# Performance work log

Measured on AMD Instinct MI355X. Metric: run time of the kernel, lower is better.

## Reference

```python
import jax, jax.numpy as jnp
import numpy as np
import math

FACTOR = 5


def setup_inputs() -> dict:
    key = jax.random.key(0)
    k1, k2, k3, k4 = jax.random.split(key, 4)
    B, L, H, D = 4, 2048, 8, 64
    sample_k = FACTOR * int(np.ceil(np.log(L)))  # 40
    queries = jax.random.normal(k1, (B, L, H, D), dtype=jnp.float32)
    keys = jax.random.normal(k2, (B, L, H, D), dtype=jnp.float32)
    values = jax.random.normal(k3, (B, L, H, D), dtype=jnp.float32)
    # per-query sampled key indices (replaces the host-side random.sample loop)
    index_sample = jax.random.randint(k4, (L, sample_k), 0, L, dtype=jnp.int64)
    return {"queries": queries, "keys": keys, "values": values,
            "index_sample": index_sample}


def reference(queries, keys, values, index_sample):
    B, L_Q, H, D = queries.shape
    L_K = keys.shape[1]
    # [B, L, H, D] -> [B, H, L, D]
    Q = jnp.transpose(queries, (0, 2, 1, 3))
    K = jnp.transpose(keys, (0, 2, 1, 3))
    V = jnp.transpose(values, (0, 2, 1, 3))

    u = min(FACTOR * int(np.ceil(np.log(L_Q))), L_Q)  # n_top

    # --- _prob_QK: sample-score-topk-gather ---
    # K_sample[b,h,i,s,e] = K[b,h,index_sample[i,s],e]  -> [B,H,L_Q,S,E]
    K_sample = K[:, :, index_sample, :]
    Q_K_sample = jnp.einsum('bhie,bhise->bhis', Q, K_sample)  # [B,H,L_Q,S]
    M = Q_K_sample.max(axis=-1) - Q_K_sample.sum(axis=-1) / L_K  # [B,H,L_Q]
    _, M_top = jax.lax.top_k(M, u)  # [B,H,u] indices of sparse queries

    Q_reduce = jnp.take_along_axis(Q, M_top[..., None], axis=2)  # [B,H,u,D]
    scores = jnp.einsum('bhue,bhke->bhuk', Q_reduce, K)  # [B,H,u,L_K]

    scale = 1.0 / math.sqrt(D)
    scores = scores * scale

    # --- initial context (mask_flag=True): causal running sum of V ---
    context = jnp.cumsum(V, axis=2)  # [B,H,L_Q,D]

    # --- ProbMask: causal mask rows gathered at M_top ---
    causal_mask = jnp.arange(L_K)[None, None, None, :] > M_top[..., None]
    scores = jnp.where(causal_mask, -jnp.inf, scores)
    attn = jax.nn.softmax(scores, axis=-1)  # [B,H,u,L_K]

    update = jnp.einsum('bhuk,bhkd->bhud', attn, V)  # [B,H,u,D]
    bi = jnp.arange(B)[:, None, None]
    hi = jnp.arange(H)[None, :, None]
    context = context.at[bi, hi, M_top].set(update)

    # back to [B, L, H, D]
    return jnp.transpose(context, (0, 2, 1, 3))
```

## Files before the change

kernel.cpp:

```cpp
#include <hip/hip_runtime.h>
#include <hip/hip_bf16.h>
#include <math.h>


#define BB 4
#define LL 2048
#define HH 8
#define DD 64
#define SS 40
#define UU 40
#define CC 64
#define LC (LL/CC)

#define KC    64
#define NCH2  8
#define UG    2
#define KSUB  4
#define KPAD  68
#define PPAD  68

#define NCSB  512
#define NMSB  (BB*LL)
#define NATB  (BB*HH*NCH2*UG)
#define NCUB  512

__global__ void k_measure_cs(const float* __restrict__ Q, const float* __restrict__ K,
                             const float* __restrict__ V, const int* __restrict__ idx,
                             float* __restrict__ M, float* __restrict__ chunkSum)
{
    __shared__ float sMax[4][8];
    __shared__ float sSum[4][8];

    int t = threadIdx.x;

    if (blockIdx.x < NCSB) {
        int w = t >> 6, lane = t & 63;
        int cI = blockIdx.x * 4 + w;
        int bh = cI >> 6, c = cI & (CC - 1);
        int b  = bh >> 3, h = bh & 7;
        int d4 = lane & 15, rs = lane >> 4;

        float4 acc = {0,0,0,0};
        int l0 = c * LC;
        for (int l = l0 + rs; l < l0 + LC; l += 4) {
            float4 v = *(const float4*)(V + (((size_t)b * LL + l) * HH + h) * DD + d4 * 4);
            acc.x += v.x; acc.y += v.y; acc.z += v.z; acc.w += v.w;
        }
        acc.x += __shfl_xor(acc.x, 16); acc.y += __shfl_xor(acc.y, 16);
        acc.z += __shfl_xor(acc.z, 16); acc.w += __shfl_xor(acc.w, 16);
        acc.x += __shfl_xor(acc.x, 32); acc.y += __shfl_xor(acc.y, 32);
        acc.z += __shfl_xor(acc.z, 32); acc.w += __shfl_xor(acc.w, 32);
        if (lane < 16)
            *(float4*)(chunkSum + ((size_t)bh * CC + c) * DD + d4 * 4) = acc;
        return;
    }

    int blk = blockIdx.x - NCSB;
    int b   = blk >> 11;
    int i   = blk & (LL - 1);
    int w    = t >> 6, lane = t & 63;
    int hg   = lane >> 4;
    int d4   = lane & 15;

    const int*   ip   = idx + (size_t)i * SS + w * 10;
    const float* Kb   = K + (size_t)b * (LL * HH * DD);
    const float* Qrow = Q + ((size_t)b * LL + i) * (HH * DD);

    float4 qa = *(const float4*)(Qrow + hg * DD + d4 * 4);
    float4 qb = *(const float4*)(Qrow + (4 + hg) * DD + d4 * 4);

    float maxa = -INFINITY, suma = 0.f;
    float maxb = -INFINITY, sumb = 0.f;

#define DOT4(q_, k_) (fmaf((q_).w, (k_).w, fmaf((q_).z, (k_).z, \
                      fmaf((q_).y, (k_).y, (q_).x * (k_).x))))

    float4 A0, B0, A1, B1;
    float4 A2, B2, A3, B3;
    {
        int k0 = ip[0], k1 = ip[1];
        const float* r0 = Kb + (size_t)k0 * (HH * DD);
        const float* r1 = Kb + (size_t)k1 * (HH * DD);
        A0 = *(const float4*)(r0 + hg * DD + d4 * 4);
        B0 = *(const float4*)(r0 + (4 + hg) * DD + d4 * 4);
        A1 = *(const float4*)(r1 + hg * DD + d4 * 4);
        B1 = *(const float4*)(r1 + (4 + hg) * DD + d4 * 4);
    }

    #pragma unroll
    for (int g = 0; g < 5; ++g) {
        if (g < 4) {
            int k2 = ip[2 * g + 2], k3 = ip[2 * g + 3];
            const float* r2 = Kb + (size_t)k2 * (HH * DD);
            const float* r3 = Kb + (size_t)k3 * (HH * DD);
            A2 = *(const float4*)(r2 + hg * DD + d4 * 4);
            B2 = *(const float4*)(r2 + (4 + hg) * DD + d4 * 4);
            A3 = *(const float4*)(r3 + hg * DD + d4 * 4);
            B3 = *(const float4*)(r3 + (4 + hg) * DD + d4 * 4);
        }
        __builtin_amdgcn_sched_barrier(0);

        float pa0 = DOT4(qa, A0), pb0 = DOT4(qb, B0);
        float pa1 = DOT4(qa, A1), pb1 = DOT4(qb, B1);
        #pragma unroll
        for (int off = 1; off < 16; off <<= 1) {
            pa0 += __shfl_xor(pa0, off);
            pb0 += __shfl_xor(pb0, off);
            pa1 += __shfl_xor(pa1, off);
            pb1 += __shfl_xor(pb1, off);
        }
        maxa = fmaxf(maxa, fmaxf(pa0, pa1));  suma += pa0 + pa1;
        maxb = fmaxf(maxb, fmaxf(pb0, pb1));  sumb += pb0 + pb1;

        A0 = A2; B0 = B2; A1 = A3; B1 = B3;
    }
#undef DOT4

    if (d4 == 0) {
        sMax[w][hg]     = maxa;  sSum[w][hg]     = suma;
        sMax[w][4 + hg] = maxb;  sSum[w][4 + hg] = sumb;
    }
    __syncthreads();

    if (t < 8) {
        float mx = sMax[0][t], sm = sSum[0][t];
        #pragma unroll
        for (int w2 = 1; w2 < 4; ++w2) {
            mx = fmaxf(mx, sMax[w2][t]);
            sm += sSum[w2][t];
        }
        M[((size_t)(b * HH + t)) * LL + i] = mx - sm * (1.0f / (float)LL);
    }
}

__global__ void k_topk(const float* __restrict__ M, int* __restrict__ topIdx)
{
    int lane = threadIdx.x;
    int bh   = blockIdx.x;
    const float* Mp = M + (size_t)bh * LL;

    unsigned k[32];
    #pragma unroll
    for (int r = 0; r < 32; ++r) {
        unsigned u = __float_as_uint(Mp[r * 64 + lane]);
        k[r] = (u & 0x80000000u) ? ~u : (u | 0x80000000u);
    }

    unsigned T = 0u;
    for (int bit = 31; bit >= 0; --bit) {
        unsigned cand = T | (1u << bit);
        int c = 0;
        #pragma unroll
        for (int r = 0; r < 32; ++r) c += (k[r] >= cand) ? 1 : 0;
        #pragma unroll
        for (int off = 1; off < 64; off <<= 1) c += __shfl_xor(c, off);
        if (c >= UU) T = cand;
    }

    int cGT = 0, cGE = 0;
    #pragma unroll
    for (int r = 0; r < 32; ++r) {
        cGT += (k[r] > T) ? 1 : 0;
        cGE += (k[r] >= T) ? 1 : 0;
    }
    #pragma unroll
    for (int off = 1; off < 64; off <<= 1) {
        cGT += __shfl_xor(cGT, off);
        cGE += __shfl_xor(cGE, off);
    }

    int need = UU - cGT;
    int X = LL;
    if (cGE - cGT != need) {
        int lo2 = 0;
        for (int bit = 10; bit >= 0; --bit) {
            int cand = lo2 | (1 << bit);
            int c = 0;
            #pragma unroll
            for (int r = 0; r < 32; ++r)
                c += (k[r] == T && (r * 64 + lane) < cand) ? 1 : 0;
            #pragma unroll
            for (int off = 1; off < 64; off <<= 1) c += __shfl_xor(c, off);
            if (c < need) lo2 = cand;
        }
        X = lo2 + 1;
    }

    unsigned inMask = 0u;
    int cnt = 0;
    #pragma unroll
    for (int r = 0; r < 32; ++r) {
        bool in = (k[r] > T) || (k[r] == T && (r * 64 + lane) < X);
        if (in) { inMask |= 1u << r; ++cnt; }
    }
    int pre = cnt;
    #pragma unroll
    for (int off = 1; off < 64; off <<= 1) {
        int v = __shfl_up(pre, off);
        if (lane >= off) pre += v;
    }
    int slot = pre - cnt;
    #pragma unroll
    for (int r = 0; r < 32; ++r) {
        if ((inMask >> r) & 1u) {
            topIdx[bh * UU + slot] = r * 64 + lane;
            ++slot;
        }
    }
}

__launch_bounds__(256, 2)
__global__ void k_attn_cum(const float* __restrict__ Q, const float* __restrict__ K,
                           const float* __restrict__ V, const int* __restrict__ topIdx,
                           float* __restrict__ Oc, float* __restrict__ Lc,
                           const float* __restrict__ chunkSum, float* __restrict__ out)
{
    __shared__ float sK[2][KC][KPAD];
    __shared__ float sV[2][KC][KPAD];
    __shared__ float sP[20][PPAD];
    __shared__ int   sPos[UU];

    int t = threadIdx.x;

    if (blockIdx.x >= NATB) {
        int w    = t >> 6, lane = t & 63;
        int cI   = (blockIdx.x - NATB) * 4 + w;
        int c    = cI & (CC - 1);
        int bh   = cI >> 6;
        int b    = bh >> 3, h = bh & 7;
        int d4   = lane & 15, s = lane >> 4;

        const float4* CS4 = (const float4*)chunkSum;
        float4 off = {0,0,0,0};
        for (int c2 = s; c2 < c; c2 += 4) {
            float4 x = CS4[((size_t)bh * CC + c2) * 16 + d4];
            off.x += x.x; off.y += x.y; off.z += x.z; off.w += x.w;
        }
        off.x += __shfl_xor(off.x, 16); off.y += __shfl_xor(off.y, 16);
        off.z += __shfl_xor(off.z, 16); off.w += __shfl_xor(off.w, 16);
        off.x += __shfl_xor(off.x, 32); off.y += __shfl_xor(off.y, 32);
        off.z += __shfl_xor(off.z, 32); off.w += __shfl_xor(off.w, 32);

        int l0 = c * LC + s * 8;
        size_t base = (((size_t)b * LL + l0) * HH + h) * DD + d4 * 4;
        const size_t stride = (size_t)HH * DD;

        float4 v[8];
        #pragma unroll
        for (int r = 0; r < 8; ++r)
            v[r] = *(const float4*)(V + base + (size_t)r * stride);
        #pragma unroll
        for (int r = 1; r < 8; ++r) {
            v[r].x += v[r-1].x; v[r].y += v[r-1].y;
            v[r].z += v[r-1].z; v[r].w += v[r-1].w;
        }

        float4 inc = v[7];
        float4 p1;
        p1.x = __shfl_up(inc.x, 16); p1.y = __shfl_up(inc.y, 16);
        p1.z = __shfl_up(inc.z, 16); p1.w = __shfl_up(inc.w, 16);
        if (s >= 1) { inc.x += p1.x; inc.y += p1.y; inc.z += p1.z; inc.w += p1.w; }
        float4 p2;
        p2.x = __shfl_up(inc.x, 32); p2.y = __shfl_up(inc.y, 32);
        p2.z = __shfl_up(inc.z, 32); p2.w = __shfl_up(inc.w, 32);
        if (s >= 2) { inc.x += p2.x; inc.y += p2.y; inc.z += p2.z; inc.w += p2.w; }

        float4 add;
        add.x = off.x + inc.x - v[7].x;
        add.y = off.y + inc.y - v[7].y;
        add.z = off.z + inc.z - v[7].z;
        add.w = off.w + inc.w - v[7].w;

        #pragma unroll
        for (int r = 0; r < 8; ++r) {
            float4 o;
            o.x = v[r].x + add.x; o.y = v[r].y + add.y;
            o.z = v[r].z + add.z; o.w = v[r].w + add.w;
            *(float4*)(out + base + (size_t)r * stride) = o;
        }
        return;
    }

    int bid = blockIdx.x;
    int bh  = bid / (NCH2 * UG);
    int rem = bid % (NCH2 * UG);
    int ch  = rem / UG, ug = rem % UG;
    int b   = bh / HH, h = bh % HH;

    if (t < UU) sPos[t] = topIdx[bh * UU + t];

    int j  = t & 63;
    int w  = t >> 6, lane = t & 63;
    int ub = __builtin_amdgcn_readfirstlane(w) * 5;

    int d4p = t & 15, tg = t >> 4;
    float4 a0 = {0,0,0,0}, a1 = {0,0,0,0};
    float den[5] = {0.f, 0.f, 0.f, 0.f, 0.f};

    const float* Kh = K + ((size_t)b * LL * HH + h) * DD;
    const float* Vh = V + ((size_t)b * LL * HH + h) * DD;

    float4 pk0, pk1, pk2, pk3, pv0, pv1, pv2, pv3;

#define ISSUE(k0_) { \
    size_t g0 = (size_t)((k0_) +  0 + tg) * (HH * DD) + d4p * 4; \
    size_t g1 = (size_t)((k0_) + 16 + tg) * (HH * DD) + d4p * 4; \
    size_t g2 = (size_t)((k0_) + 32 + tg) * (HH * DD) + d4p * 4; \
    size_t g3 = (size_t)((k0_) + 48 + tg) * (HH * DD) + d4p * 4; \
    pk0 = *(const float4*)(Kh + g0); pv0 = *(const float4*)(Vh + g0); \
    pk1 = *(const float4*)(Kh + g1); pv1 = *(const float4*)(Vh + g1); \
    pk2 = *(const float4*)(Kh + g2); pv2 = *(const float4*)(Vh + g2); \
    pk3 = *(const float4*)(Kh + g3); pv3 = *(const float4*)(Vh + g3); \
}
#define COMMIT(buf_) { \
    *(float4*)&sK[buf_][ 0 + tg][d4p * 4] = pk0; *(float4*)&sV[buf_][ 0 + tg][d4p * 4] = pv0; \
    *(float4*)&sK[buf_][16 + tg][d4p * 4] = pk1; *(float4*)&sV[buf_][16 + tg][d4p * 4] = pv1; \
    *(float4*)&sK[buf_][32 + tg][d4p * 4] = pk2; *(float4*)&sV[buf_][32 + tg][d4p * 4] = pv2; \
    *(float4*)&sK[buf_][48 + tg][d4p * 4] = pk3; *(float4*)&sV[buf_][48 + tg][d4p * 4] = pv3; \
}

    int k0base = ch * KSUB * KC;
    ISSUE(k0base);
    COMMIT(0);
    __syncthreads();

    #pragma unroll
    for (int sub = 0; sub < KSUB; ++sub) {
        int cur = sub & 1;
        int k0  = k0base + sub * KC;

        if (sub + 1 < KSUB) ISSUE(k0 + KC);

        int jg = k0 + j;
        {
            int p0 = __builtin_amdgcn_readfirstlane(sPos[ug * 20 + ub + 0]);
            int p1 = __builtin_amdgcn_readfirstlane(sPos[ug * 20 + ub + 1]);
            int p2 = __builtin_amdgcn_readfirstlane(sPos[ug * 20 + ub + 2]);
            int p3 = __builtin_amdgcn_readfirstlane(sPos[ug * 20 + ub + 3]);
            int p4 = __builtin_amdgcn_readfirstlane(sPos[ug * 20 + ub + 4]);
            const float* q0 = Q + (((size_t)b * LL + p0) * HH + h) * DD;
            const float* q1 = Q + (((size_t)b * LL + p1) * HH + h) * DD;
            const float* q2 = Q + (((size_t)b * LL + p2) * HH + h) * DD;
            const float* q3 = Q + (((size_t)b * LL + p3) * HH + h) * DD;
            const float* q4 = Q + (((size_t)b * LL + p4) * HH + h) * DD;
            float c0 = 0.f, c1 = 0.f, c2 = 0.f, c3 = 0.f, c4 = 0.f;
            #pragma unroll
            for (int d4 = 0; d4 < 16; ++d4) {
                float4 kk = *(const float4*)&sK[cur][j][d4 * 4];
                int d = d4 * 4;
                c0 = fmaf(kk.x, q0[d], c0); c0 = fmaf(kk.y, q0[d+1], c0);
                c0 = fmaf(kk.z, q0[d+2], c0); c0 = fmaf(kk.w, q0[d+3], c0);
                c1 = fmaf(kk.x, q1[d], c1); c1 = fmaf(kk.y, q1[d+1], c1);
                c1 = fmaf(kk.z, q1[d+2], c1); c1 = fmaf(kk.w, q1[d+3], c1);
                c2 = fmaf(kk.x, q2[d], c2); c2 = fmaf(kk.y, q2[d+1], c2);
                c2 = fmaf(kk.z, q2[d+2], c2); c2 = fmaf(kk.w, q2[d+3], c2);
                c3 = fmaf(kk.x, q3[d], c3); c3 = fmaf(kk.y, q3[d+1], c3);
                c3 = fmaf(kk.z, q3[d+2], c3); c3 = fmaf(kk.w, q3[d+3], c3);
                c4 = fmaf(kk.x, q4[d], c4); c4 = fmaf(kk.y, q4[d+1], c4);
                c4 = fmaf(kk.z, q4[d+2], c4); c4 = fmaf(kk.w, q4[d+3], c4);
            }
            float e0 = (jg > p0) ? 0.f : __expf(c0 * 0.125f);
            float e1 = (jg > p1) ? 0.f : __expf(c1 * 0.125f);
            float e2 = (jg > p2) ? 0.f : __expf(c2 * 0.125f);
            float e3 = (jg > p3) ? 0.f : __expf(c3 * 0.125f);
            float e4 = (jg > p4) ? 0.f : __expf(c4 * 0.125f);
            sP[ub + 0][j] = e0;
            sP[ub + 1][j] = e1;
            sP[ub + 2][j] = e2;
            sP[ub + 3][j] = e3;
            sP[ub + 4][j] = e4;
            #pragma unroll
            for (int off = 1; off < 64; off <<= 1) {
                e0 += __shfl_xor(e0, off);
                e1 += __shfl_xor(e1, off);
                e2 += __shfl_xor(e2, off);
                e3 += __shfl_xor(e3, off);
                e4 += __shfl_xor(e4, off);
            }
            den[0] += e0; den[1] += e1; den[2] += e2; den[3] += e3; den[4] += e4;
        }
        __syncthreads();

        if (sub + 1 < KSUB) {
            if (cur == 0) { COMMIT(1); } else { COMMIT(0); }
        }

        #pragma unroll 4
        for (int j4 = 0; j4 < KC / 4; ++j4) {
            float4 pj0 = *(const float4*)&sP[tg][j4 * 4];
            float4 pj1 = (tg < 4) ? *(const float4*)&sP[16 + tg][j4 * 4]
                                  : (float4){0,0,0,0};
            float4 va = *(const float4*)&sV[cur][j4 * 4 + 0][d4p * 4];
            float4 vb = *(const float4*)&sV[cur][j4 * 4 + 1][d4p * 4];
            float4 vc = *(const float4*)&sV[cur][j4 * 4 + 2][d4p * 4];
            float4 vd = *(const float4*)&sV[cur][j4 * 4 + 3][d4p * 4];
            a0.x = fmaf(pj0.x, va.x, fmaf(pj0.y, vb.x, fmaf(pj0.z, vc.x, fmaf(pj0.w, vd.x, a0.x))));
            a0.y = fmaf(pj0.x, va.y, fmaf(pj0.y, vb.y, fmaf(pj0.z, vc.y, fmaf(pj0.w, vd.y, a0.y))));
            a0.z = fmaf(pj0.x, va.z, fmaf(pj0.y, vb.z, fmaf(pj0.z, vc.z, fmaf(pj0.w, vd.z, a0.z))));
            a0.w = fmaf(pj0.x, va.w, fmaf(pj0.y, vb.w, fmaf(pj0.z, vc.w, fmaf(pj0.w, vd.w, a0.w))));
            a1.x = fmaf(pj1.x, va.x, fmaf(pj1.y, vb.x, fmaf(pj1.z, vc.x, fmaf(pj1.w, vd.x, a1.x))));
            a1.y = fmaf(pj1.x, va.y, fmaf(pj1.y, vb.y, fmaf(pj1.z, vc.y, fmaf(pj1.w, vd.y, a1.y))));
            a1.z = fmaf(pj1.x, va.z, fmaf(pj1.y, vb.z, fmaf(pj1.z, vc.z, fmaf(pj1.w, vd.z, a1.z))));
            a1.w = fmaf(pj1.x, va.w, fmaf(pj1.y, vb.w, fmaf(pj1.z, vc.w, fmaf(pj1.w, vd.w, a1.w))));
        }
        __syncthreads();
    }
#undef ISSUE
#undef COMMIT

    if (lane == 0) {
        int base = (bh * NCH2 + ch) * UU + ug * 20 + ub;
        Lc[base + 0] = den[0]; Lc[base + 1] = den[1]; Lc[base + 2] = den[2];
        Lc[base + 3] = den[3]; Lc[base + 4] = den[4];
    }
    {
        int u0g = ug * 20 + tg;
        size_t o0 = ((size_t)(bh * NCH2 + ch) * UU + u0g) * DD + d4p * 4;
        *(float4*)(Oc + o0) = a0;
        if (tg < 4) {
            int u1g = ug * 20 + 16 + tg;
            size_t o1 = ((size_t)(bh * NCH2 + ch) * UU + u1g) * DD + d4p * 4;
            *(float4*)(Oc + o1) = a1;
        }
    }
}

__global__ void k_finalize(const float* __restrict__ Oc, const float* __restrict__ Lc,
                           const int* __restrict__ topIdx, float* __restrict__ out)
{
    int bh = blockIdx.x;
    int b  = bh / HH, h = bh % HH;
    int t  = threadIdx.x;
    int d  = t & 63, w = t >> 6;
    for (int i = 0; i < 10; ++i) {
        int u = w * 10 + i;
        int pos = topIdx[bh * UU + u];
        float num = 0.f, den = 0.f;
        #pragma unroll
        for (int c = 0; c < NCH2; ++c) {
            num += Oc[((size_t)(bh * NCH2 + c) * UU + u) * DD + d];
            den += Lc[(bh * NCH2 + c) * UU + u];
        }
        out[(((size_t)b * LL + pos) * HH + h) * DD + d] = num / den;
    }
}

extern "C" void kernel_launch(void* const* d_in, const int* in_sizes, int n_in,
                              void* d_out, int out_size, void* d_ws, size_t ws_size,
                              hipStream_t stream)
{
    const float* Q   = (const float*)d_in[0];
    const float* K   = (const float*)d_in[1];
    const float* V   = (const float*)d_in[2];
    const int*   idx = (const int*)d_in[3];
    float* out = (float*)d_out;

    float* M        = (float*)d_ws;
    int*   topIdx   = (int*)(M + (size_t)BB * HH * LL);
    float* Oc       = (float*)(topIdx + BB * HH * UU);
    float* Lc       = Oc + (size_t)BB * HH * NCH2 * UU * DD;
    float* chunkSum = Lc + BB * HH * NCH2 * UU;

    k_measure_cs<<<NCSB + NMSB, 256, 0, stream>>>(Q, K, V, idx, M, chunkSum);
    k_topk      <<<BB * HH,      64, 0, stream>>>(M, topIdx);
    k_attn_cum  <<<NATB + NCUB, 256, 0, stream>>>(Q, K, V, topIdx, Oc, Lc, chunkSum, out);
    k_finalize  <<<BB * HH,     256, 0, stream>>>(Oc, Lc, topIdx, out);
}
```

Baseline: 178.2 us.

## Fuse top-k and finalize into preceding kernels via last-block atomic counters

Removes the separate top-k and finalize kernel launches. The last measure block for each batch, found with an atomic counter, runs the top-k for that batch's heads. The last attention/cumsum block for each (b,h) does the cross-chunk reduction. This cuts launch gaps and tail idle time, at the cost of a memset, extra fences and atomics in every block, and a serial top-k tail running on a single block per batch.

```diff
diff --git a/kernel.cpp b/kernel.cpp
--- a/kernel.cpp
+++ b/kernel.cpp
@@ -24,121 +24,10 @@
 #define NATB  (BB*HH*NCH2*UG)
 #define NCUB  512
 
-__global__ void k_measure_cs(const float* __restrict__ Q, const float* __restrict__ K,
-                             const float* __restrict__ V, const int* __restrict__ idx,
-                             float* __restrict__ M, float* __restrict__ chunkSum)
+__device__ __forceinline__ void topk_wave(const float* __restrict__ Mp,
+                                          int* __restrict__ topIdx,
+                                          int bh, int lane)
 {
-    __shared__ float sMax[4][8];
-    __shared__ float sSum[4][8];
-
-    int t = threadIdx.x;
-
-    if (blockIdx.x < NCSB) {
-        int w = t >> 6, lane = t & 63;
-        int cI = blockIdx.x * 4 + w;
-        int bh = cI >> 6, c = cI & (CC - 1);
-        int b  = bh >> 3, h = bh & 7;
-        int d4 = lane & 15, rs = lane >> 4;
-
-        float4 acc = {0,0,0,0};
-        int l0 = c * LC;
-        for (int l = l0 + rs; l < l0 + LC; l += 4) {
-            float4 v = *(const float4*)(V + (((size_t)b * LL + l) * HH + h) * DD + d4 * 4);
-            acc.x += v.x; acc.y += v.y; acc.z += v.z; acc.w += v.w;
-        }
-        acc.x += __shfl_xor(acc.x, 16); acc.y += __shfl_xor(acc.y, 16);
-        acc.z += __shfl_xor(acc.z, 16); acc.w += __shfl_xor(acc.w, 16);
-        acc.x += __shfl_xor(acc.x, 32); acc.y += __shfl_xor(acc.y, 32);
-        acc.z += __shfl_xor(acc.z, 32); acc.w += __shfl_xor(acc.w, 32);
-        if (lane < 16)
-            *(float4*)(chunkSum + ((size_t)bh * CC + c) * DD + d4 * 4) = acc;
-        return;
-    }
-
-    int blk = blockIdx.x - NCSB;
-    int b   = blk >> 11;
-    int i   = blk & (LL - 1);
-    int w    = t >> 6, lane = t & 63;
-    int hg   = lane >> 4;
-    int d4   = lane & 15;
-
-    const int*   ip   = idx + (size_t)i * SS + w * 10;
-    const float* Kb   = K + (size_t)b * (LL * HH * DD);
-    const float* Qrow = Q + ((size_t)b * LL + i) * (HH * DD);
-
-    float4 qa = *(const float4*)(Qrow + hg * DD + d4 * 4);
-    float4 qb = *(const float4*)(Qrow + (4 + hg) * DD + d4 * 4);
-
-    float maxa = -INFINITY, suma = 0.f;
-    float maxb = -INFINITY, sumb = 0.f;
-
-#define DOT4(q_, k_) (fmaf((q_).w, (k_).w, fmaf((q_).z, (k_).z, \
-                      fmaf((q_).y, (k_).y, (q_).x * (k_).x))))
-
-    float4 A0, B0, A1, B1;
-    float4 A2, B2, A3, B3;
-    {
-        int k0 = ip[0], k1 = ip[1];
-        const float* r0 = Kb + (size_t)k0 * (HH * DD);
-        const float* r1 = Kb + (size_t)k1 * (HH * DD);
-        A0 = *(const float4*)(r0 + hg * DD + d4 * 4);
-        B0 = *(const float4*)(r0 + (4 + hg) * DD + d4 * 4);
-        A1 = *(const float4*)(r1 + hg * DD + d4 * 4);
-        B1 = *(const float4*)(r1 + (4 + hg) * DD + d4 * 4);
-    }
-
-    #pragma unroll
-    for (int g = 0; g < 5; ++g) {
-        if (g < 4) {
-            int k2 = ip[2 * g + 2], k3 = ip[2 * g + 3];
-            const float* r2 = Kb + (size_t)k2 * (HH * DD);
-            const float* r3 = Kb + (size_t)k3 * (HH * DD);
-            A2 = *(const float4*)(r2 + hg * DD + d4 * 4);
-            B2 = *(const float4*)(r2 + (4 + hg) * DD + d4 * 4);
-            A3 = *(const float4*)(r3 + hg * DD + d4 * 4);
-            B3 = *(const float4*)(r3 + (4 + hg) * DD + d4 * 4);
-        }
-        __builtin_amdgcn_sched_barrier(0);
-
-        float pa0 = DOT4(qa, A0), pb0 = DOT4(qb, B0);
-        float pa1 = DOT4(qa, A1), pb1 = DOT4(qb, B1);
-        #pragma unroll
-        for (int off = 1; off < 16; off <<= 1) {
-            pa0 += __shfl_xor(pa0, off);
-            pb0 += __shfl_xor(pb0, off);
-            pa1 += __shfl_xor(pa1, off);
-            pb1 += __shfl_xor(pb1, off);
-        }
-        maxa = fmaxf(maxa, fmaxf(pa0, pa1));  suma += pa0 + pa1;
-        maxb = fmaxf(maxb, fmaxf(pb0, pb1));  sumb += pb0 + pb1;
-
-        A0 = A2; B0 = B2; A1 = A3; B1 = B3;
-    }
-#undef DOT4
-
-    if (d4 == 0) {
-        sMax[w][hg]     = maxa;  sSum[w][hg]     = suma;
-        sMax[w][4 + hg] = maxb;  sSum[w][4 + hg] = sumb;
-    }
-    __syncthreads();
-
-    if (t < 8) {
-        float mx = sMax[0][t], sm = sSum[0][t];
-        #pragma unroll
-        for (int w2 = 1; w2 < 4; ++w2) {
-            mx = fmaxf(mx, sMax[w2][t]);
-            sm += sSum[w2][t];
-        }
-        M[((size_t)(b * HH + t)) * LL + i] = mx - sm * (1.0f / (float)LL);
-    }
-}
-
-__global__ void k_topk(const float* __restrict__ M, int* __restrict__ topIdx)
-{
-    int lane = threadIdx.x;
-    int bh   = blockIdx.x;
-    const float* Mp = M + (size_t)bh * LL;
-
     unsigned k[32];
     #pragma unroll
     for (int r = 0; r < 32; ++r) {
@@ -209,22 +98,151 @@
     }
 }
 
+__global__ void k_measure_cs(const float* __restrict__ Q, const float* __restrict__ K,
+                             const float* __restrict__ V, const int* __restrict__ idx,
+                             float* __restrict__ M, float* __restrict__ chunkSum,
+                             int* __restrict__ topIdx, int* __restrict__ cntA)
+{
+    __shared__ float sMax[4][8];
+    __shared__ float sSum[4][8];
+    __shared__ int   sLastA;
+
+    int t = threadIdx.x;
+
+    if (blockIdx.x < NCSB) {
+        int w = t >> 6, lane = t & 63;
+        int cI = blockIdx.x * 4 + w;
+        int bh = cI >> 6, c = cI & (CC - 1);
+        int b  = bh >> 3, h = bh & 7;
+        int d4 = lane & 15, rs = lane >> 4;
+
+        float4 acc = {0,0,0,0};
+        int l0 = c * LC;
+        for (int l = l0 + rs; l < l0 + LC; l += 4) {
+            float4 v = *(const float4*)(V + (((size_t)b * LL + l) * HH + h) * DD + d4 * 4);
+            acc.x += v.x; acc.y += v.y; acc.z += v.z; acc.w += v.w;
+        }
+        acc.x += __shfl_xor(acc.x, 16); acc.y += __shfl_xor(acc.y, 16);
+        acc.z += __shfl_xor(acc.z, 16); acc.w += __shfl_xor(acc.w, 16);
+        acc.x += __shfl_xor(acc.x, 32); acc.y += __shfl_xor(acc.y, 32);
+        acc.z += __shfl_xor(acc.z, 32); acc.w += __shfl_xor(acc.w, 32);
+        if (lane < 16)
+            *(float4*)(chunkSum + ((size_t)bh * CC + c) * DD + d4 * 4) = acc;
+        return;
+    }
+
+    int blk = blockIdx.x - NCSB;
+    int b   = blk >> 11;
+    int i   = blk & (LL - 1);
+    int w    = t >> 6, lane = t & 63;
+    int hg   = lane >> 4;
+    int d4   = lane & 15;
+
+    const int*   ip   = idx + (size_t)i * SS + w * 10;
+    const float* Kb   = K + (size_t)b * (LL * HH * DD);
+    const float* Qrow = Q + ((size_t)b * LL + i) * (HH * DD);
+
+    float4 qa = *(const float4*)(Qrow + hg * DD + d4 * 4);
+    float4 qb = *(const float4*)(Qrow + (4 + hg) * DD + d4 * 4);
+
+    float maxa = -INFINITY, suma = 0.f;
+    float maxb = -INFINITY, sumb = 0.f;
+
+#define DOT4(q_, k_) (fmaf((q_).w, (k_).w, fmaf((q_).z, (k_).z, \
+                      fmaf((q_).y, (k_).y, (q_).x * (k_).x))))
+
+    float4 A0, B0, A1, B1;
+    float4 A2, B2, A3, B3;
+    {
+        int k0 = ip[0], k1 = ip[1];
+        const float* r0 = Kb + (size_t)k0 * (HH * DD);
+        const float* r1 = Kb + (size_t)k1 * (HH * DD);
+        A0 = *(const float4*)(r0 + hg * DD + d4 * 4);
+        B0 = *(const float4*)(r0 + (4 + hg) * DD + d4 * 4);
+        A1 = *(const float4*)(r1 + hg * DD + d4 * 4);
+        B1 = *(const float4*)(r1 + (4 + hg) * DD + d4 * 4);
+    }
+
+    #pragma unroll
+    for (int g = 0; g < 5; ++g) {
+        if (g < 4) {
+            int k2 = ip[2 * g + 2], k3 = ip[2 * g + 3];
+            const float* r2 = Kb + (size_t)k2 * (HH * DD);
+            const float* r3 = Kb + (size_t)k3 * (HH * DD);
+            A2 = *(const float4*)(r2 + hg * DD + d4 * 4);
+            B2 = *(const float4*)(r2 + (4 + hg) * DD + d4 * 4);
+            A3 = *(const float4*)(r3 + hg * DD + d4 * 4);
+            B3 = *(const float4*)(r3 + (4 + hg) * DD + d4 * 4);
+        }
+        __builtin_amdgcn_sched_barrier(0);
+
+        float pa0 = DOT4(qa, A0), pb0 = DOT4(qb, B0);
+        float pa1 = DOT4(qa, A1), pb1 = DOT4(qb, B1);
+        #pragma unroll
+        for (int off = 1; off < 16; off <<= 1) {
+            pa0 += __shfl_xor(pa0, off);
+            pb0 += __shfl_xor(pb0, off);
+            pa1 += __shfl_xor(pa1, off);
+            pb1 += __shfl_xor(pb1, off);
+        }
+        maxa = fmaxf(maxa, fmaxf(pa0, pa1));  suma += pa0 + pa1;
+        maxb = fmaxf(maxb, fmaxf(pb0, pb1));  sumb += pb0 + pb1;
+
+        A0 = A2; B0 = B2; A1 = A3; B1 = B3;
+    }
+#undef DOT4
+
+    if (d4 == 0) {
+        sMax[w][hg]     = maxa;  sSum[w][hg]     = suma;
+        sMax[w][4 + hg] = maxb;  sSum[w][4 + hg] = sumb;
+    }
+    __syncthreads();
+
+    if (t < 8) {
+        float mx = sMax[0][t], sm = sSum[0][t];
+        #pragma unroll
+        for (int w2 = 1; w2 < 4; ++w2) {
+            mx = fmaxf(mx, sMax[w2][t]);
+            sm += sSum[w2][t];
+        }
+        M[((size_t)(b * HH + t)) * LL + i] = mx - sm * (1.0f / (float)LL);
+    }
+
+    if (w == 0) __threadfence();
+    __syncthreads();
+    if (t == 0) sLastA = (atomicAdd(&cntA[b], 1) == LL - 1) ? 1 : 0;
+    __syncthreads();
+    if (sLastA) {
+        __threadfence();
+        #pragma unroll
+        for (int rep = 0; rep < 2; ++rep) {
+            int bh2 = b * HH + rep * 4 + w;
+            topk_wave(M + (size_t)bh2 * LL, topIdx, bh2, lane);
+        }
+    }
+}
+
 __launch_bounds__(256, 2)
-__global__ void k_attn_cum(const float* __restrict__ Q, const float* __restrict__ K,
-                           const float* __restrict__ V, const int* __restrict__ topIdx,
-                           float* __restrict__ Oc, float* __restrict__ Lc,
-                           const float* __restrict__ chunkSum, float* __restrict__ out)
+__global__ void k_attn_cum_fin(const float* __restrict__ Q, const float* __restrict__ K,
+                               const float* __restrict__ V, const int* __restrict__ topIdx,
+                               float* __restrict__ Oc, float* __restrict__ Lc,
+                               const float* __restrict__ chunkSum, float* __restrict__ out,
+                               int* __restrict__ cntC)
 {
     __shared__ float sK[2][KC][KPAD];
     __shared__ float sV[2][KC][KPAD];
     __shared__ float sP[20][PPAD];
     __shared__ int   sPos[UU];
-
-    int t = threadIdx.x;
-
-    if (blockIdx.x >= NATB) {
+    __shared__ int   sLastC;
+
+    int t   = threadIdx.x;
+    int blk = blockIdx.x;
+    int mybh;
+
+    if (blk >= NATB) {
+        mybh = (blk - NATB) >> 4;
         int w    = t >> 6, lane = t & 63;
-        int cI   = (blockIdx.x - NATB) * 4 + w;
+        int cI   = (blk - NATB) * 4 + w;
         int c    = cI & (CC - 1);
         int bh   = cI >> 6;
         int b    = bh >> 3, h = bh & 7;
@@ -278,29 +296,28 @@
             o.z = v[r].z + add.z; o.w = v[r].w + add.w;
             *(float4*)(out + base + (size_t)r * stride) = o;
         }
-        return;
-    }
-
-    int bid = blockIdx.x;
-    int bh  = bid / (NCH2 * UG);
-    int rem = bid % (NCH2 * UG);
-    int ch  = rem / UG, ug = rem % UG;
-    int b   = bh / HH, h = bh % HH;
-
-    if (t < UU) sPos[t] = topIdx[bh * UU + t];
-
-    int j  = t & 63;
-    int w  = t >> 6, lane = t & 63;
-    int ub = __builtin_amdgcn_readfirstlane(w) * 5;
-
-    int d4p = t & 15, tg = t >> 4;
-    float4 a0 = {0,0,0,0}, a1 = {0,0,0,0};
-    float den[5] = {0.f, 0.f, 0.f, 0.f, 0.f};
-
-    const float* Kh = K + ((size_t)b * LL * HH + h) * DD;
-    const float* Vh = V + ((size_t)b * LL * HH + h) * DD;
-
-    float4 pk0, pk1, pk2, pk3, pv0, pv1, pv2, pv3;
+    } else {
+        int bid = blk;
+        int bh  = bid / (NCH2 * UG);
+        int rem = bid % (NCH2 * UG);
+        int ch  = rem / UG, ug = rem % UG;
+        int b   = bh / HH, h = bh % HH;
+        mybh = bh;
+
+        if (t < UU) sPos[t] = topIdx[bh * UU + t];
+
+        int j  = t & 63;
+        int w  = t >> 6, lane = t & 63;
+        int ub = __builtin_amdgcn_readfirstlane(w) * 5;
+
+        int d4p = t & 15, tg = t >> 4;
+        float4 a0 = {0,0,0,0}, a1 = {0,0,0,0};
+        float den[5] = {0.f, 0.f, 0.f, 0.f, 0.f};
+
+        const float* Kh = K + ((size_t)b * LL * HH + h) * DD;
+        const float* Vh = V + ((size_t)b * LL * HH + h) * DD;
+
+        float4 pk0, pk1, pk2, pk3, pv0, pv1, pv2, pv3;
 
 #define ISSUE(k0_) { \
     size_t g0 = (size_t)((k0_) +  0 + tg) * (HH * DD) + d4p * 4; \
@@ -319,129 +336,131 @@
     *(float4*)&sK[buf_][48 + tg][d4p * 4] = pk3; *(float4*)&sV[buf_][48 + tg][d4p * 4] = pv3; \
 }
 
-    int k0base = ch * KSUB * KC;
-    ISSUE(k0base);
-    COMMIT(0);
-    __syncthreads();
-
-    #pragma unroll
-    for (int sub = 0; sub < KSUB; ++sub) {
-        int cur = sub & 1;
-        int k0  = k0base + sub * KC;
-
-        if (sub + 1 < KSUB) ISSUE(k0 + KC);
-
-        int jg = k0 + j;
-        {
-            int p0 = __builtin_amdgcn_readfirstlane(sPos[ug * 20 + ub + 0]);
-            int p1 = __builtin_amdgcn_readfirstlane(sPos[ug * 20 + ub + 1]);
-            int p2 = __builtin_amdgcn_readfirstlane(sPos[ug * 20 + ub + 2]);
-            int p3 = __builtin_amdgcn_readfirstlane(sPos[ug * 20 + ub + 3]);
-            int p4 = __builtin_amdgcn_readfirstlane(sPos[ug * 20 + ub + 4]);
-            const float* q0 = Q + (((size_t)b * LL + p0) * HH + h) * DD;
-            const float* q1 = Q + (((size_t)b * LL + p1) * HH + h) * DD;
-            const float* q2 = Q + (((size_t)b * LL + p2) * HH + h) * DD;
-            const float* q3 = Q + (((size_t)b * LL + p3) * HH + h) * DD;
-            const float* q4 = Q + (((size_t)b * LL + p4) * HH + h) * DD;
-            float c0 = 0.f, c1 = 0.f, c2 = 0.f, c3 = 0.f, c4 = 0.f;
-            #pragma unroll
-            for (int d4 = 0; d4 < 16; ++d4) {
-                float4 kk = *(const float4*)&sK[cur][j][d4 * 4];
-                int d = d4 * 4;
-                c0 = fmaf(kk.x, q0[d], c0); c0 = fmaf(kk.y, q0[d+1], c0);
-                c0 = fmaf(kk.z, q0[d+2], c0); c0 = fmaf(kk.w, q0[d+3], c0);
-                c1 = fmaf(kk.x, q1[d], c1); c1 = fmaf(kk.y, q1[d+1], c1);
-                c1 = fmaf(kk.z, q1[d+2], c1); c1 = fmaf(kk.w, q1[d+3], c1);
-                c2 = fmaf(kk.x, q2[d], c2); c2 = fmaf(kk.y, q2[d+1], c2);
-                c2 = fmaf(kk.z, q2[d+2], c2); c2 = fmaf(kk.w, q2[d+3], c2);
-                c3 = fmaf(kk.x, q3[d], c3); c3 = fmaf(kk.y, q3[d+1], c3);
-                c3 = fmaf(kk.z, q3[d+2], c3); c3 = fmaf(kk.w, q3[d+3], c3);
-                c4 = fmaf(kk.x, q4[d], c4); c4 = fmaf(kk.y, q4[d+1], c4);
-                c4 = fmaf(kk.z, q4[d+2], c4); c4 = fmaf(kk.w, q4[d+3], c4);
+        int k0base = ch * KSUB * KC;
+        ISSUE(k0base);
+        COMMIT(0);
+        __syncthreads();
+
+        #pragma unroll
+        for (int sub = 0; sub < KSUB; ++sub) {
+            int cur = sub & 1;
+            int k0  = k0base + sub * KC;
+
+            if (sub + 1 < KSUB) ISSUE(k0 + KC);
+
+            int jg = k0 + j;
+            {
+                int p0 = __builtin_amdgcn_readfirstlane(sPos[ug * 20 + ub + 0]);
+                int p1 = __builtin_amdgcn_readfirstlane(sPos[ug * 20 + ub + 1]);
+                int p2 = __builtin_amdgcn_readfirstlane(sPos[ug * 20 + ub + 2]);
+                int p3 = __builtin_amdgcn_readfirstlane(sPos[ug * 20 + ub + 3]);
+                int p4 = __builtin_amdgcn_readfirstlane(sPos[ug * 20 + ub + 4]);
+                const float* q0 = Q + (((size_t)b * LL + p0) * HH + h) * DD;
+                const float* q1 = Q + (((size_t)b * LL + p1) * HH + h) * DD;
+                const float* q2 = Q + (((size_t)b * LL + p2) * HH + h) * DD;
+                const float* q3 = Q + (((size_t)b * LL + p3) * HH + h) * DD;
+                const float* q4 = Q + (((size_t)b * LL + p4) * HH + h) * DD;
+                float c0 = 0.f, c1 = 0.f, c2 = 0.f, c3 = 0.f, c4 = 0.f;
+                #pragma unroll
+                for (int d4 = 0; d4 < 16; ++d4) {
+                    float4 kk = *(const float4*)&sK[cur][j][d4 * 4];
+                    int d = d4 * 4;
+                    c0 = fmaf(kk.x, q0[d], c0); c0 = fmaf(kk.y, q0[d+1], c0);
+                    c0 = fmaf(kk.z, q0[d+2], c0); c0 = fmaf(kk.w, q0[d+3], c0);
+                    c1 = fmaf(kk.x, q1[d], c1); c1 = fmaf(kk.y, q1[d+1], c1);
+                    c1 = fmaf(kk.z, q1[d+2], c1); c1 = fmaf(kk.w, q1[d+3], c1);
+                    c2 = fmaf(kk.x, q2[d], c2); c2 = fmaf(kk.y, q2[d+1], c2);
+                    c2 = fmaf(kk.z, q2[d+2], c2); c2 = fmaf(kk.w, q2[d+3], c2);
+                    c3 = fmaf(kk.x, q3[d], c3); c3 = fmaf(kk.y, q3[d+1], c3);
+                    c3 = fmaf(kk.z, q3[d+2], c3); c3 = fmaf(kk.w, q3[d+3], c3);
+                    c4 = fmaf(kk.x, q4[d], c4); c4 = fmaf(kk.y, q4[d+1], c4);
+                    c4 = fmaf(kk.z, q4[d+2], c4); c4 = fmaf(kk.w, q4[d+3], c4);
+                }
+                float e0 = (jg > p0) ? 0.f : __expf(c0 * 0.125f);
+                float e1 = (jg > p1) ? 0.f : __expf(c1 * 0.125f);
+                float e2 = (jg > p2) ? 0.f : __expf(c2 * 0.125f);
+                float e3 = (jg > p3) ? 0.f : __expf(c3 * 0.125f);
+                float e4 = (jg > p4) ? 0.f : __expf(c4 * 0.125f);
+                sP[ub + 0][j] = e0;
+                sP[ub + 1][j] = e1;
+                sP[ub + 2][j] = e2;
+                sP[ub + 3][j] = e3;
+                sP[ub + 4][j] = e4;
+                #pragma unroll
+                for (int off = 1; off < 64; off <<= 1) {
+                    e0 += __shfl_xor(e0, off);
+                    e1 += __shfl_xor(e1, off);
+                    e2 += __shfl_xor(e2, off);
+                    e3 += __shfl_xor(e3, off);
+                    e4 += __shfl_xor(e4, off);
+                }
+                den[0] += e0; den[1] += e1; den[2] += e2; den[3] += e3; den[4] += e4;
             }
-            float e0 = (jg > p0) ? 0.f : __expf(c0 * 0.125f);
-            float e1 = (jg > p1) ? 0.f : __expf(c1 * 0.125f);
-            float e2 = (jg > p2) ? 0.f : __expf(c2 * 0.125f);
-            float e3 = (jg > p3) ? 0.f : __expf(c3 * 0.125f);
-            float e4 = (jg > p4) ? 0.f : __expf(c4 * 0.125f);
-            sP[ub + 0][j] = e0;
-            sP[ub + 1][j] = e1;
-            sP[ub + 2][j] = e2;
-            sP[ub + 3][j] = e3;
-            sP[ub + 4][j] = e4;
-            #pragma unroll
-            for (int off = 1; off < 64; off <<= 1) {
-                e0 += __shfl_xor(e0, off);
-                e1 += __shfl_xor(e1, off);
-                e2 += __shfl_xor(e2, off);
-                e3 += __shfl_xor(e3, off);
-                e4 += __shfl_xor(e4, off);
+            __syncthreads();
+
+            if (sub + 1 < KSUB) {
+                if (cur == 0) { COMMIT(1); } else { COMMIT(0); }
             }
-            den[0] += e0; den[1] += e1; den[2] += e2; den[3] += e3; den[4] += e4;
-        }
-        __syncthreads();
-
-        if (sub + 1 < KSUB) {
-            if (cur == 0) { COMMIT(1); } else { COMMIT(0); }
-        }
-
-        #pragma unroll 4
-        for (int j4 = 0; j4 < KC / 4; ++j4) {
-            float4 pj0 = *(const float4*)&sP[tg][j4 * 4];
-            float4 pj1 = (tg < 4) ? *(const float4*)&sP[16 + tg][j4 * 4]
-                                  : (float4){0,0,0,0};
-            float4 va = *(const float4*)&sV[cur][j4 * 4 + 0][d4p * 4];
-            float4 vb = *(const float4*)&sV[cur][j4 * 4 + 1][d4p * 4];
-            float4 vc = *(const float4*)&sV[cur][j4 * 4 + 2][d4p * 4];
-            float4 vd = *(const float4*)&sV[cur][j4 * 4 + 3][d4p * 4];
-            a0.x = fmaf(pj0.x, va.x, fmaf(pj0.y, vb.x, fmaf(pj0.z, vc.x, fmaf(pj0.w, vd.x, a0.x))));
-            a0.y = fmaf(pj0.x, va.y, fmaf(pj0.y, vb.y, fmaf(pj0.z, vc.y, fmaf(pj0.w, vd.y, a0.y))));
-            a0.z = fmaf(pj0.x, va.z, fmaf(pj0.y, vb.z, fmaf(pj0.z, vc.z, fmaf(pj0.w, vd.z, a0.z))));
-            a0.w = fmaf(pj0.x, va.w, fmaf(pj0.y, vb.w, fmaf(pj0.z, vc.w, fmaf(pj0.w, vd.w, a0.w))));
-            a1.x = fmaf(pj1.x, va.x, fmaf(pj1.y, vb.x, fmaf(pj1.z, vc.x, fmaf(pj1.w, vd.x, a1.x))));
-            a1.y = fmaf(pj1.x, va.y, fmaf(pj1.y, vb.y, fmaf(pj1.z, vc.y, fmaf(pj1.w, vd.y, a1.y))));
-            a1.z = fmaf(pj1.x, va.z, fmaf(pj1.y, vb.z, fmaf(pj1.z, vc.z, fmaf(pj1.w, vd.z, a1.z))));
-            a1.w = fmaf(pj1.x, va.w, fmaf(pj1.y, vb.w, fmaf(pj1.z, vc.w, fmaf(pj1.w, vd.w, a1.w))));
-        }
-        __syncthreads();
-    }
+
+            #pragma unroll 4
+            for (int j4 = 0; j4 < KC / 4; ++j4) {
+                float4 pj0 = *(const float4*)&sP[tg][j4 * 4];
+                float4 pj1 = (tg < 4) ? *(const float4*)&sP[16 + tg][j4 * 4]
+                                      : (float4){0,0,0,0};
+                float4 va = *(const float4*)&sV[cur][j4 * 4 + 0][d4p * 4];
+                float4 vb = *(const float4*)&sV[cur][j4 * 4 + 1][d4p * 4];
+                float4 vc = *(const float4*)&sV[cur][j4 * 4 + 2][d4p * 4];
+                float4 vd = *(const float4*)&sV[cur][j4 * 4 + 3][d4p * 4];
+                a0.x = fmaf(pj0.x, va.x, fmaf(pj0.y, vb.x, fmaf(pj0.z, vc.x, fmaf(pj0.w, vd.x, a0.x))));
+                a0.y = fmaf(pj0.x, va.y, fmaf(pj0.y, vb.y, fmaf(pj0.z, vc.y, fmaf(pj0.w, vd.y, a0.y))));
+                a0.z = fmaf(pj0.x, va.z, fmaf(pj0.y, vb.z, fmaf(pj0.z, vc.z, fmaf(pj0.w, vd.z, a0.z))));
+                a0.w = fmaf(pj0.x, va.w, fmaf(pj0.y, vb.w, fmaf(pj0.z, vc.w, fmaf(pj0.w, vd.w, a0.w))));
+                a1.x = fmaf(pj1.x, va.x, fmaf(pj1.y, vb.x, fmaf(pj1.z, vc.x, fmaf(pj1.w, vd.x, a1.x))));
+                a1.y = fmaf(pj1.x, va.y, fmaf(pj1.y, vb.y, fmaf(pj1.z, vc.y, fmaf(pj1.w, vd.y, a1.y))));
+                a1.z = fmaf(pj1.x, va.z, fmaf(pj1.y, vb.z, fmaf(pj1.z, vc.z, fmaf(pj1.w, vd.z, a1.z))));
+                a1.w = fmaf(pj1.x, va.w, fmaf(pj1.y, vb.w, fmaf(pj1.z, vc.w, fmaf(pj1.w, vd.w, a1.w))));
+            }
+            __syncthreads();
+        }
 #undef ISSUE
 #undef COMMIT
 
-    if (lane == 0) {
-        int base = (bh * NCH2 + ch) * UU + ug * 20 + ub;
-        Lc[base + 0] = den[0]; Lc[base + 1] = den[1]; Lc[base + 2] = den[2];
-        Lc[base + 3] = den[3]; Lc[base + 4] = den[4];
-    }
-    {
-        int u0g = ug * 20 + tg;
-        size_t o0 = ((size_t)(bh * NCH2 + ch) * UU + u0g) * DD + d4p * 4;
-        *(float4*)(Oc + o0) = a0;
-        if (tg < 4) {
-            int u1g = ug * 20 + 16 + tg;
-            size_t o1 = ((size_t)(bh * NCH2 + ch) * UU + u1g) * DD + d4p * 4;
-            *(float4*)(Oc + o1) = a1;
-        }
-    }
-}
-
-__global__ void k_finalize(const float* __restrict__ Oc, const float* __restrict__ Lc,
-                           const int* __restrict__ topIdx, float* __restrict__ out)
-{
-    int bh = blockIdx.x;
-    int b  = bh / HH, h = bh % HH;
-    int t  = threadIdx.x;
-    int d  = t & 63, w = t >> 6;
-    for (int i = 0; i < 10; ++i) {
-        int u = w * 10 + i;
-        int pos = topIdx[bh * UU + u];
-        float num = 0.f, den = 0.f;
-        #pragma unroll
-        for (int c = 0; c < NCH2; ++c) {
-            num += Oc[((size_t)(bh * NCH2 + c) * UU + u) * DD + d];
-            den += Lc[(bh * NCH2 + c) * UU + u];
-        }
-        out[(((size_t)b * LL + pos) * HH + h) * DD + d] = num / den;
+        if (lane == 0) {
+            int base = (bh * NCH2 + ch) * UU + ug * 20 + ub;
+            Lc[base + 0] = den[0]; Lc[base + 1] = den[1]; Lc[base + 2] = den[2];
+            Lc[base + 3] = den[3]; Lc[base + 4] = den[4];
+        }
+        {
+            int u0g = ug * 20 + tg;
+            size_t o0 = ((size_t)(bh * NCH2 + ch) * UU + u0g) * DD + d4p * 4;
+            *(float4*)(Oc + o0) = a0;
+            if (tg < 4) {
+                int u1g = ug * 20 + 16 + tg;
+                size_t o1 = ((size_t)(bh * NCH2 + ch) * UU + u1g) * DD + d4p * 4;
+                *(float4*)(Oc + o1) = a1;
+            }
+        }
+    }
+
+    __threadfence();
+    __syncthreads();
+    if (t == 0) sLastC = (atomicAdd(&cntC[mybh], 1) == 31) ? 1 : 0;
+    __syncthreads();
+    if (sLastC) {
+        __threadfence();
+        int b  = mybh / HH, h = mybh % HH;
+        int d  = t & 63, w2 = t >> 6;
+        for (int i2 = 0; i2 < 10; ++i2) {
+            int u = w2 * 10 + i2;
+            int pos = topIdx[mybh * UU + u];
+            float num = 0.f, den2 = 0.f;
+            #pragma unroll
+            for (int c = 0; c < NCH2; ++c) {
+                num  += Oc[((size_t)(mybh * NCH2 + c) * UU + u) * DD + d];
+                den2 += Lc[(mybh * NCH2 + c) * UU + u];
+            }
+            out[(((size_t)b * LL + pos) * HH + h) * DD + d] = num / den2;
+        }
     }
 }
 
@@ -460,9 +479,13 @@
     float* Oc       = (float*)(topIdx + BB * HH * UU);
     float* Lc       = Oc + (size_t)BB * HH * NCH2 * UU * DD;
     float* chunkSum = Lc + BB * HH * NCH2 * UU;
-
-    k_measure_cs<<<NCSB + NMSB, 256, 0, stream>>>(Q, K, V, idx, M, chunkSum);
-    k_topk      <<<BB * HH,      64, 0, stream>>>(M, topIdx);
-    k_attn_cum  <<<NATB + NCUB, 256, 0, stream>>>(Q, K, V, topIdx, Oc, Lc, chunkSum, out);
-    k_finalize  <<<BB * HH,     256, 0, stream>>>(Oc, Lc, topIdx, out);
-}
+    int*   cnt      = (int*)(chunkSum + (size_t)BB * HH * CC * DD);
+    int*   cntA     = cnt;
+    int*   cntC     = cnt + BB;
+
+    hipMemsetAsync(cnt, 0, (BB + BB * HH) * sizeof(int), stream);
+    k_measure_cs  <<<NCSB + NMSB, 256, 0, stream>>>(Q, K, V, idx, M, chunkSum,
+                                                    topIdx, cntA);
+    k_attn_cum_fin<<<NATB + NCUB, 256, 0, stream>>>(Q, K, V, topIdx, Oc, Lc,
+                                                    chunkSum, out, cntC);
+}
```

New measurement: 576.4 us. 224% more time.
